# Kernel tuning notes

Measured on AMD Instinct MI355X. Metric: run time of the kernel, lower is better.

Reference implementation:

```python
import jax, jax.numpy as jnp
import numpy as np

N_NODES = 100000
N_EDGES = 1600000
IN_FEATS = 128
HEADS = 4
OUT_FEATS = 32
NEG_SLOPE = 0.2


def setup_inputs() -> dict:
    key = jax.random.key(0)
    ks = jax.random.split(key, 7)
    x = jax.random.normal(ks[0], (N_NODES, IN_FEATS), dtype=jnp.float32)
    fc_w = jax.random.normal(ks[1], (HEADS * OUT_FEATS, IN_FEATS), dtype=jnp.float32) * (1.0 / np.sqrt(IN_FEATS))
    attn_l = jax.random.normal(ks[2], (HEADS, OUT_FEATS), dtype=jnp.float32) * (1.0 / np.sqrt(OUT_FEATS))
    attn_r = jax.random.normal(ks[3], (HEADS, OUT_FEATS), dtype=jnp.float32) * (1.0 / np.sqrt(OUT_FEATS))
    bias = jnp.zeros((HEADS * OUT_FEATS,), dtype=jnp.float32)
    src = jax.random.randint(ks[4], (N_EDGES,), 0, N_NODES, dtype=jnp.int64 if jax.config.jax_enable_x64 else jnp.int32)
    dst = jax.random.randint(ks[5], (N_EDGES,), 0, N_NODES, dtype=jnp.int64 if jax.config.jax_enable_x64 else jnp.int32)
    return {"x": x, "fc_w": fc_w, "attn_l": attn_l, "attn_r": attn_r, "bias": bias, "src": src, "dst": dst}


def reference(x, fc_w, attn_l, attn_r, bias, src, dst):
    """DGL GATConv (feat_drop=attn_drop=0, residual identity since in==H*D,
    allow_zero_in_degree=True, activation=None), then concat heads."""
    N = x.shape[0]
    H, D = attn_l.shape
    # linear projection: [N, H, D]
    feat = (x @ fc_w.T).reshape(N, H, D)
    # per-node attention halves: [N, H]
    el = jnp.einsum('nhd,hd->nh', feat, attn_l)
    er = jnp.einsum('nhd,hd->nh', feat, attn_r)
    # per-edge score with leaky relu: [E, H]
    e = el[src] + er[dst]
    e = jnp.where(e > 0, e, NEG_SLOPE * e)
    # edge softmax grouped by destination node
    emax = jax.ops.segment_max(e, dst, num_segments=N)          # [N, H]
    ee = jnp.exp(e - emax[dst])                                  # [E, H]
    denom = jax.ops.segment_sum(ee, dst, num_segments=N)        # [N, H]
    a = ee / jnp.maximum(denom[dst], jnp.float32(1e-38))         # [E, H]
    # weighted message + scatter aggregate: [N, H, D]
    msg = feat[src] * a[:, :, None]
    rst = jax.ops.segment_sum(msg, dst, num_segments=N)
    # residual (identity since in_feats == H*D) + bias
    rst = rst + x.reshape(N, H, D) + bias.reshape(1, H, D)
    # concat heads
    return rst.reshape(N, H * D)
```

## Files before the change

kernel.cpp:

```cpp
#include <hip/hip_runtime.h>
#include <math.h>

#define NEG_SLOPE 0.2f
#define PB 256
#define BKT_SHIFT 8
#define WSLICES 8

typedef __attribute__((ext_vector_type(8))) short bf16x8;
typedef __attribute__((ext_vector_type(4))) float f32x4;

__device__ __forceinline__ unsigned bf16_rne(float f) {
  unsigned u = __float_as_uint(f);
  return (u + 0x7fff + ((u >> 16) & 1)) >> 16;
}

__device__ __forceinline__ float lrelu_exp(float v) {
  v = v > 0.f ? v : NEG_SLOPE * v;
  return __expf(v);
}

__device__ __forceinline__ void local_blk_scan(const int* __restrict__ blk_sums,
                                               int* s_blk_off, int nb, int t) {
  if (t < 64) {
    const int v = (t < nb) ? blk_sums[t] : 0;
    int incl = v;
#pragma unroll
    for (int d = 1; d < 64; d <<= 1) {
      const int o = __shfl_up(incl, d);
      if (t >= d) incl += o;
    }
    s_blk_off[t] = incl - v;
  }
}

__global__ __launch_bounds__(256) void gemm_feat_attn(
    const float* __restrict__ x, const unsigned* __restrict__ fc_wb,
    const float* __restrict__ attn_l, const float* __restrict__ attn_r,
    unsigned* __restrict__ featb, float* __restrict__ el,
    float* __restrict__ er, int N)
{
  __shared__ __align__(16) unsigned w_lds[128 * 68];
  const int t = threadIdx.x;
  const int row_base = blockIdx.x * 64;

  {
    const uint4* fb4 = reinterpret_cast<const uint4*>(fc_wb);
#pragma unroll
    for (int k = 0; k < 8; ++k) {
      const int i4 = t + k * 256;
      const uint4 v = fb4[i4];
      const int row = i4 >> 4;
      unsigned* d = &w_lds[row * 68 + (i4 & 15) * 4];
      d[0] = v.x; d[1] = v.y; d[2] = v.z; d[3] = v.w;
    }
  }

  const int w = t >> 6;
  const int l = t & 63;
  const int cl = l & 15;
  const int g = l >> 4;

  const int arow = min(row_base + w * 16 + cl, N - 1);
  const float* __restrict__ xp = x + (size_t)arow * 128;
  bf16x8 a_frag[4];
#pragma unroll
  for (int ks = 0; ks < 4; ++ks) {
    const float4 v0 = *reinterpret_cast<const float4*>(xp + ks * 32 + g * 8);
    const float4 v1 =
        *reinterpret_cast<const float4*>(xp + ks * 32 + g * 8 + 4);
    uint4 uu;
    uu.x = bf16_rne(v0.x) | (bf16_rne(v0.y) << 16);
    uu.y = bf16_rne(v0.z) | (bf16_rne(v0.w) << 16);
    uu.z = bf16_rne(v1.x) | (bf16_rne(v1.y) << 16);
    uu.w = bf16_rne(v1.z) | (bf16_rne(v1.w) << 16);
    a_frag[ks] = *reinterpret_cast<bf16x8*>(&uu);
  }
  __syncthreads();

  f32x4 acc[8];
#pragma unroll
  for (int ct = 0; ct < 8; ++ct) acc[ct] = (f32x4){0.f, 0.f, 0.f, 0.f};

#pragma unroll
  for (int ct = 0; ct < 8; ++ct) {
#pragma unroll
    for (int ks = 0; ks < 4; ++ks) {
      const bf16x8 b_frag = *reinterpret_cast<const bf16x8*>(
          &w_lds[(ct * 16 + cl) * 68 + ks * 16 + g * 4]);
      acc[ct] = __builtin_amdgcn_mfma_f32_16x16x32_bf16(a_frag[ks], b_frag,
                                                        acc[ct], 0, 0, 0);
    }
  }

#pragma unroll
  for (int ct = 0; ct < 8; ++ct) {
#pragma unroll
    for (int r = 0; r < 4; ++r) {
      const float v = acc[ct][r];
      const float vn = __shfl_xor(v, 1);
      const int node = row_base + w * 16 + g * 4 + r;
      if ((cl & 1) == 0 && node < N) {
        featb[(size_t)node * 64 + ct * 8 + (cl >> 1)] =
            bf16_rne(v) | (bf16_rne(vn) << 16);
      }
    }
  }

  float al_lo[4], al_hi[4], ar_lo[4], ar_hi[4];
#pragma unroll
  for (int h = 0; h < 4; ++h) {
    al_lo[h] = attn_l[h * 32 + cl];
    al_hi[h] = attn_l[h * 32 + 16 + cl];
    ar_lo[h] = attn_r[h * 32 + cl];
    ar_hi[h] = attn_r[h * 32 + 16 + cl];
  }
#pragma unroll
  for (int r = 0; r < 4; ++r) {
    const int node = row_base + w * 16 + g * 4 + r;
#pragma unroll
    for (int h = 0; h < 4; ++h) {
      float pl = acc[2 * h][r] * al_lo[h] + acc[2 * h + 1][r] * al_hi[h];
      float pr = acc[2 * h][r] * ar_lo[h] + acc[2 * h + 1][r] * ar_hi[h];
#pragma unroll
      for (int d = 1; d < 16; d <<= 1) {
        pl += __shfl_xor(pl, d);
        pr += __shfl_xor(pr, d);
      }
      if (cl == 0 && node < N) {
        el[(size_t)node * 4 + h] = pl;
        er[(size_t)node * 4 + h] = pr;
      }
    }
  }
}

__global__ __launch_bounds__(256) void hist_bucket(const int* __restrict__ dst,
                                                   int* __restrict__ hist,
                                                   const float* __restrict__ fc_w,
                                                   unsigned* __restrict__ fc_wb,
                                                   int E, int NB, int chunk) {
  __shared__ int h[512];
  const int k = blockIdx.x, t = threadIdx.x;
  if (k < 32) {
    const int i = k * 256 + t;
    const float2 v = reinterpret_cast<const float2*>(fc_w)[i];
    fc_wb[i] = bf16_rne(v.x) | (bf16_rne(v.y) << 16);
  }
  for (int i = t; i < NB; i += 256) h[i] = 0;
  __syncthreads();
  const int beg = k * chunk, end = min(E, beg + chunk);
  for (int e = beg + t; e < end; e += 256)
    atomicAdd(&h[dst[e] >> BKT_SHIFT], 1);
  __syncthreads();
  for (int i = t; i < NB; i += 256) hist[i * PB + k] = h[i];
}

__global__ __launch_bounds__(256) void scan_a(const int* __restrict__ deg,
                                              int* __restrict__ offs,
                                              int* __restrict__ blk_sums,
                                              int n) {
  __shared__ int wsum[4];
  const int b = blockIdx.x, t = threadIdx.x;
  const int base = b * 2048 + t * 8;
  int v[8];
  int s = 0;
#pragma unroll
  for (int j = 0; j < 8; ++j) {
    v[j] = s;
    const int d = (base + j < n) ? deg[base + j] : 0;
    s += d;
  }
  const int lane = t & 63;
  int incl = s;
#pragma unroll
  for (int d = 1; d < 64; d <<= 1) {
    const int o = __shfl_up(incl, d);
    if (lane >= d) incl += o;
  }
  const int w = t >> 6;
  if (lane == 63) wsum[w] = incl;
  __syncthreads();
  int woff = 0;
  for (int ww = 0; ww < w; ++ww) woff += wsum[ww];
  const int thr_excl = woff + incl - s;
#pragma unroll
  for (int j = 0; j < 8; ++j)
    if (base + j < n) offs[base + j] = thr_excl + v[j];
  if (t == 255) blk_sums[b] = woff + incl;
}

__global__ __launch_bounds__(256) void part_scatter(
    const int* __restrict__ src, const int* __restrict__ dst,
    const int* __restrict__ hscan, const int* __restrict__ blk_sums,
    unsigned* __restrict__ part, int E, int NB, int chunk, int nb) {
  __shared__ int cur[512];
  __shared__ int s_blk_off[64];
  const int k = blockIdx.x, t = threadIdx.x;
  local_blk_scan(blk_sums, s_blk_off, nb, t);
  __syncthreads();
  for (int i = t; i < NB; i += 256) {
    const int m = i * PB + k;
    cur[i] = hscan[m] + s_blk_off[m >> 11];
  }
  __syncthreads();
  const int beg = k * chunk, end = min(E, beg + chunk);
  for (int e = beg + t; e < end; e += 256) {
    const int d = dst[e];
    const int b = d >> BKT_SHIFT;
    const int pos = atomicAdd(&cur[b], 1);
    part[pos] = (unsigned)src[e] |
                ((unsigned)(d & ((1 << BKT_SHIFT) - 1)) << 20);
  }
}

__global__ __launch_bounds__(256) void build_csr(
    const unsigned* __restrict__ part, const int* __restrict__ hscan,
    const int* __restrict__ blk_sums, int* __restrict__ node_offs,
    unsigned* __restrict__ csr, int N, int E, int NB, int nb) {
  __shared__ int cnt[256];
  __shared__ int wtot[4];
  __shared__ int s_blk_off[64];
  const int b = blockIdx.x, t = threadIdx.x;
  local_blk_scan(blk_sums, s_blk_off, nb, t);
  if (t < 256) cnt[t] = 0;
  __syncthreads();
  const int m0 = b * PB;
  const int bbase = hscan[m0] + s_blk_off[m0 >> 11];
  int bend = E;
  if (b + 1 < NB) {
    const int m1 = (b + 1) * PB;
    bend = hscan[m1] + s_blk_off[m1 >> 11];
  }
  const int node0 = b << BKT_SHIFT;
  for (int p = bbase + t; p < bend; p += 256)
    atomicAdd(&cnt[part[p] >> 20], 1);
  __syncthreads();
  const int a0 = cnt[t];
  int incl = a0;
#pragma unroll
  for (int d1 = 1; d1 < 64; d1 <<= 1) {
    const int o = __shfl_up(incl, d1);
    if ((t & 63) >= d1) incl += o;
  }
  const int w = t >> 6;
  if ((t & 63) == 63) wtot[w] = incl;
  __syncthreads();
  int woff = 0;
  for (int ww = 0; ww < w; ++ww) woff += wtot[ww];
  const int e0 = woff + incl - a0;
  cnt[t] = e0;
  if (node0 + t < N) node_offs[node0 + t] = bbase + e0;
  if (b == NB - 1 && t == 0) node_offs[N] = E;
  __syncthreads();
  for (int p = bbase + t; p < bend; p += 256) {
    const unsigned v = part[p];
    const int lpos = atomicAdd(&cnt[v >> 20], 1);
    csr[bbase + lpos] = v;
  }
}

__global__ __launch_bounds__(256) void compute_w(
    const unsigned* __restrict__ csr, const int* __restrict__ hscan,
    const int* __restrict__ blk_sums, const float* __restrict__ el,
    const float* __restrict__ er, uint2* __restrict__ wsb, int E, int NB,
    int nb) {
  __shared__ int s_blk_off[64];
  const int b = blockIdx.x / WSLICES;
  const int sl = blockIdx.x - b * WSLICES;
  local_blk_scan(blk_sums, s_blk_off, nb, (int)threadIdx.x);
  __syncthreads();
  const int m0 = b * PB;
  const int bbase = hscan[m0] + s_blk_off[m0 >> 11];
  int bend = E;
  if (b + 1 < NB) {
    const int m1 = (b + 1) * PB;
    bend = hscan[m1] + s_blk_off[m1 >> 11];
  }
  const int node0 = b << BKT_SHIFT;
  const int len = bend - bbase;
  const int per = (len + WSLICES - 1) / WSLICES;
  const int s0 = bbase + sl * per;
  const int s1 = min(bend, s0 + per);
  for (int pos = s0 + (int)threadIdx.x; pos < s1; pos += 256) {
    const unsigned v = csr[pos];
    const unsigned s = v & 0xFFFFFu;
    const unsigned ld = v >> 20;
    const float4 l4 = *reinterpret_cast<const float4*>(el + s * 4);
    const float4 r4 =
        *reinterpret_cast<const float4*>(er + (unsigned)(node0 + ld) * 4);
    uint2 u;
    u.x = bf16_rne(lrelu_exp(l4.x + r4.x)) |
          (bf16_rne(lrelu_exp(l4.y + r4.y)) << 16);
    u.y = bf16_rne(lrelu_exp(l4.z + r4.z)) |
          (bf16_rne(lrelu_exp(l4.w + r4.w)) << 16);
    wsb[pos] = u;
  }
}

__global__ __launch_bounds__(256) void agg_kernel(
    const uint2* __restrict__ featb2, const unsigned* __restrict__ csr,
    const unsigned short* __restrict__ wsb_us, const float* __restrict__ x,
    const float* __restrict__ bias, const int* __restrict__ node_offs,
    float* __restrict__ out, int N, int E)
{
  const int n = (int)((blockIdx.x * (size_t)blockDim.x + threadIdx.x) >> 6);
  if (n >= N) return;
  const unsigned lane = threadIdx.x & 63;
  const unsigned half = lane >> 5;
  const unsigned li = lane & 31;
  const unsigned hh = li >> 3;
  const unsigned short* __restrict__ wp = wsb_us + hh;
  const int beg = node_offs[n];
  const int end = node_offs[n + 1];
  const int nfull = (end - beg) >> 3;

  float a0 = 0.f, a1 = 0.f, a2 = 0.f, a3 = 0.f, ds = 0.f;
  int p = beg;
  for (int gi = 0; gi < nfull; ++gi, p += 8) {
    unsigned pk[4]; unsigned wu[4]; uint2 fv[4];
#pragma unroll
    for (int i = 0; i < 4; ++i) pk[i] = csr[(unsigned)p + 2 * i + half];
#pragma unroll
    for (int i = 0; i < 4; ++i)
      wu[i] = wp[((unsigned)p + 2 * i + half) * 4];
#pragma unroll
    for (int i = 0; i < 4; ++i)
      fv[i] = featb2[(pk[i] & 0xFFFFFu) * 32 + li];
#pragma unroll
    for (int i = 0; i < 4; ++i) {
      const float w = __uint_as_float(wu[i] << 16);
      a0 = fmaf(w, __uint_as_float(fv[i].x << 16), a0);
      a1 = fmaf(w, __uint_as_float(fv[i].x & 0xffff0000u), a1);
      a2 = fmaf(w, __uint_as_float(fv[i].y << 16), a2);
      a3 = fmaf(w, __uint_as_float(fv[i].y & 0xffff0000u), a3);
      ds += w;
    }
  }
  if (p < end) {
    const int last = end - 1;
#pragma unroll
    for (int i = 0; i < 4; ++i) {
      const int e = p + 2 * i + (int)half;
      const unsigned ec = (unsigned)min(e, last);
      const unsigned pk = csr[ec];
      float w = __uint_as_float((unsigned)wp[ec * 4] << 16);
      if (e > last) w = 0.f;
      const uint2 fv = featb2[(pk & 0xFFFFFu) * 32 + li];
      a0 = fmaf(w, __uint_as_float(fv.x << 16), a0);
      a1 = fmaf(w, __uint_as_float(fv.x & 0xffff0000u), a1);
      a2 = fmaf(w, __uint_as_float(fv.y << 16), a2);
      a3 = fmaf(w, __uint_as_float(fv.y & 0xffff0000u), a3);
      ds += w;
    }
  }

  a0 += __shfl_xor(a0, 32);
  a1 += __shfl_xor(a1, 32);
  a2 += __shfl_xor(a2, 32);
  a3 += __shfl_xor(a3, 32);
  ds += __shfl_xor(ds, 32);

  if (half == 0) {
    const float inv = 1.f / fmaxf(ds, 1e-38f);
    const float4 xr = ((const float4*)x)[(unsigned)n * 32 + li];
    const float4 br = ((const float4*)bias)[li];
    float4 o;
    o.x = fmaf(a0, inv, xr.x + br.x);
    o.y = fmaf(a1, inv, xr.y + br.y);
    o.z = fmaf(a2, inv, xr.z + br.z);
    o.w = fmaf(a3, inv, xr.w + br.w);
    ((float4*)out)[(unsigned)n * 32 + li] = o;
  }
}

extern "C" void kernel_launch(void* const* d_in, const int* in_sizes, int n_in,
                              void* d_out, int out_size, void* d_ws,
                              size_t ws_size, hipStream_t stream) {
  const float* x      = (const float*)d_in[0];
  const float* fc_w   = (const float*)d_in[1];
  const float* attn_l = (const float*)d_in[2];
  const float* attn_r = (const float*)d_in[3];
  const float* bias   = (const float*)d_in[4];
  const int*   src    = (const int*)d_in[5];
  const int*   dst    = (const int*)d_in[6];
  const int N = in_sizes[0] / 128;
  const int E = in_sizes[5];
  float* out = (float*)d_out;

  const int NB = (N + 255) >> 8;
  const int M = NB * PB;
  const int chunk = (E + PB - 1) / PB;
  const int nb = (M + 2047) / 2048;

  char* ws = (char*)d_ws;
  size_t off = 0;
  auto alloc = [&](size_t bytes) {
    void* p = ws + off;
    off += (bytes + 255) & ~(size_t)255;
    return p;
  };
  unsigned* featb   = (unsigned*)alloc((size_t)N * 128 * 2);
  unsigned* fc_wb   = (unsigned*)alloc(128 * 64 * 4);
  float* el         = (float*)alloc((size_t)N * 4 * 4);
  float* er         = (float*)alloc((size_t)N * 4 * 4);
  int*   hist       = (int*)alloc((size_t)M * 4);
  int*   hscan      = (int*)alloc((size_t)(M + 1) * 4);
  int*   node_offs  = (int*)alloc((size_t)(N + 1) * 4);
  int*   blk_sums   = (int*)alloc(256);
  unsigned* part    = (unsigned*)alloc((size_t)E * 4);
  unsigned* csr     = (unsigned*)alloc((size_t)E * 4);
  uint2* wsb        = (uint2*)alloc((size_t)E * 8);

  hist_bucket<<<PB, 256, 0, stream>>>(dst, hist, fc_w, fc_wb, E, NB, chunk);
  gemm_feat_attn<<<(N + 63) / 64, 256, 0, stream>>>(x, fc_wb, attn_l, attn_r,
                                                    featb, el, er, N);
  scan_a<<<nb, 256, 0, stream>>>(hist, hscan, blk_sums, M);
  part_scatter<<<PB, 256, 0, stream>>>(src, dst, hscan, blk_sums, part, E,
                                       NB, chunk, nb);
  build_csr<<<NB, 256, 0, stream>>>(part, hscan, blk_sums, node_offs, csr, N,
                                    E, NB, nb);
  compute_w<<<NB * WSLICES, 256, 0, stream>>>(csr, hscan, blk_sums, el, er,
                                              wsb, E, NB, nb);
  agg_kernel<<<(N + 3) / 4, 256, 0, stream>>>((const uint2*)featb, csr,
                                              (const unsigned short*)wsb, x,
                                              bias, node_offs, out, N, E);
}
```

Measured before the change: 159.7 us.

## Fuse edge-weight computation into CSR build and widen aggregation feature loads

Removes the separate compute_w kernel by computing the bf16 exp-weights inside build_csr, which now runs with 512 threads per block and re-reads csr after a barrier. The aggregation kernel switches from 32-lane uint2 feature loads (2 edges per wave step) to 16-lane uint4 loads (4 edges per step), with an extra shuffle stage for the reduction. This saves one launch plus the global re-read of bucket offsets and reduces load instructions per edge. In exchange, build_csr gets less parallelism per bucket (391 blocks instead of 3128 for the weight pass), and the accumulators in aggregation use more registers.

```diff
diff --git a/kernel.cpp b/kernel.cpp
--- a/kernel.cpp
+++ b/kernel.cpp
@@ -4,7 +4,6 @@
 #define NEG_SLOPE 0.2f
 #define PB 256
 #define BKT_SHIFT 8
-#define WSLICES 8
 
 typedef __attribute__((ext_vector_type(8))) short bf16x8;
 typedef __attribute__((ext_vector_type(4))) float f32x4;
@@ -213,10 +212,12 @@
   }
 }
 
-__global__ __launch_bounds__(256) void build_csr(
+__global__ __launch_bounds__(512) void build_csr(
     const unsigned* __restrict__ part, const int* __restrict__ hscan,
-    const int* __restrict__ blk_sums, int* __restrict__ node_offs,
-    unsigned* __restrict__ csr, int N, int E, int NB, int nb) {
+    const int* __restrict__ blk_sums, const float* __restrict__ el,
+    const float* __restrict__ er, int* __restrict__ node_offs,
+    unsigned* __restrict__ csr, uint2* __restrict__ wsb,
+    int N, int E, int NB, int nb) {
   __shared__ int cnt[256];
   __shared__ int wtot[4];
   __shared__ int s_blk_off[64];
@@ -232,57 +233,39 @@
     bend = hscan[m1] + s_blk_off[m1 >> 11];
   }
   const int node0 = b << BKT_SHIFT;
-  for (int p = bbase + t; p < bend; p += 256)
+  for (int p = bbase + t; p < bend; p += 512)
     atomicAdd(&cnt[part[p] >> 20], 1);
   __syncthreads();
-  const int a0 = cnt[t];
-  int incl = a0;
-#pragma unroll
-  for (int d1 = 1; d1 < 64; d1 <<= 1) {
-    const int o = __shfl_up(incl, d1);
-    if ((t & 63) >= d1) incl += o;
-  }
-  const int w = t >> 6;
-  if ((t & 63) == 63) wtot[w] = incl;
-  __syncthreads();
-  int woff = 0;
-  for (int ww = 0; ww < w; ++ww) woff += wtot[ww];
-  const int e0 = woff + incl - a0;
-  cnt[t] = e0;
-  if (node0 + t < N) node_offs[node0 + t] = bbase + e0;
-  if (b == NB - 1 && t == 0) node_offs[N] = E;
-  __syncthreads();
-  for (int p = bbase + t; p < bend; p += 256) {
+  int a0 = 0, incl = 0;
+  if (t < 256) {
+    a0 = cnt[t];
+    incl = a0;
+#pragma unroll
+    for (int d1 = 1; d1 < 64; d1 <<= 1) {
+      const int o = __shfl_up(incl, d1);
+      if ((t & 63) >= d1) incl += o;
+    }
+    if ((t & 63) == 63) wtot[t >> 6] = incl;
+  }
+  __syncthreads();
+  if (t < 256) {
+    const int w = t >> 6;
+    int woff = 0;
+    for (int ww = 0; ww < w; ++ww) woff += wtot[ww];
+    const int e0 = woff + incl - a0;
+    cnt[t] = e0;
+    if (node0 + t < N) node_offs[node0 + t] = bbase + e0;
+    if (b == NB - 1 && t == 0) node_offs[N] = E;
+  }
+  __syncthreads();
+  for (int p = bbase + t; p < bend; p += 512) {
     const unsigned v = part[p];
     const int lpos = atomicAdd(&cnt[v >> 20], 1);
     csr[bbase + lpos] = v;
   }
-}
-
-__global__ __launch_bounds__(256) void compute_w(
-    const unsigned* __restrict__ csr, const int* __restrict__ hscan,
-    const int* __restrict__ blk_sums, const float* __restrict__ el,
-    const float* __restrict__ er, uint2* __restrict__ wsb, int E, int NB,
-    int nb) {
-  __shared__ int s_blk_off[64];
-  const int b = blockIdx.x / WSLICES;
-  const int sl = blockIdx.x - b * WSLICES;
-  local_blk_scan(blk_sums, s_blk_off, nb, (int)threadIdx.x);
-  __syncthreads();
-  const int m0 = b * PB;
-  const int bbase = hscan[m0] + s_blk_off[m0 >> 11];
-  int bend = E;
-  if (b + 1 < NB) {
-    const int m1 = (b + 1) * PB;
-    bend = hscan[m1] + s_blk_off[m1 >> 11];
-  }
-  const int node0 = b << BKT_SHIFT;
-  const int len = bend - bbase;
-  const int per = (len + WSLICES - 1) / WSLICES;
-  const int s0 = bbase + sl * per;
-  const int s1 = min(bend, s0 + per);
-  for (int pos = s0 + (int)threadIdx.x; pos < s1; pos += 256) {
-    const unsigned v = csr[pos];
+  __syncthreads();
+  for (int p = bbase + t; p < bend; p += 512) {
+    const unsigned v = csr[p];
     const unsigned s = v & 0xFFFFFu;
     const unsigned ld = v >> 20;
     const float4 l4 = *reinterpret_cast<const float4*>(el + s * 4);
@@ -293,12 +276,12 @@
           (bf16_rne(lrelu_exp(l4.y + r4.y)) << 16);
     u.y = bf16_rne(lrelu_exp(l4.z + r4.z)) |
           (bf16_rne(lrelu_exp(l4.w + r4.w)) << 16);
-    wsb[pos] = u;
+    wsb[p] = u;
   }
 }
 
 __global__ __launch_bounds__(256) void agg_kernel(
-    const uint2* __restrict__ featb2, const unsigned* __restrict__ csr,
+    const uint4* __restrict__ featb4, const unsigned* __restrict__ csr,
     const unsigned short* __restrict__ wsb_us, const float* __restrict__ x,
     const float* __restrict__ bias, const int* __restrict__ node_offs,
     float* __restrict__ out, int N, int E)
@@ -306,70 +289,90 @@
   const int n = (int)((blockIdx.x * (size_t)blockDim.x + threadIdx.x) >> 6);
   if (n >= N) return;
   const unsigned lane = threadIdx.x & 63;
-  const unsigned half = lane >> 5;
-  const unsigned li = lane & 31;
-  const unsigned hh = li >> 3;
+  const unsigned q = lane >> 4;
+  const unsigned li = lane & 15;
+  const unsigned hh = li >> 2;
   const unsigned short* __restrict__ wp = wsb_us + hh;
   const int beg = node_offs[n];
   const int end = node_offs[n + 1];
   const int nfull = (end - beg) >> 3;
 
-  float a0 = 0.f, a1 = 0.f, a2 = 0.f, a3 = 0.f, ds = 0.f;
+  float a0 = 0.f, a1 = 0.f, a2 = 0.f, a3 = 0.f;
+  float a4 = 0.f, a5 = 0.f, a6 = 0.f, a7 = 0.f, ds = 0.f;
   int p = beg;
   for (int gi = 0; gi < nfull; ++gi, p += 8) {
-    unsigned pk[4]; unsigned wu[4]; uint2 fv[4];
-#pragma unroll
-    for (int i = 0; i < 4; ++i) pk[i] = csr[(unsigned)p + 2 * i + half];
-#pragma unroll
-    for (int i = 0; i < 4; ++i)
-      wu[i] = wp[((unsigned)p + 2 * i + half) * 4];
-#pragma unroll
-    for (int i = 0; i < 4; ++i)
-      fv[i] = featb2[(pk[i] & 0xFFFFFu) * 32 + li];
-#pragma unroll
-    for (int i = 0; i < 4; ++i) {
+    unsigned pk[2]; unsigned wu[2]; uint4 fv[2];
+#pragma unroll
+    for (int i = 0; i < 2; ++i) pk[i] = csr[(unsigned)p + 4 * i + q];
+#pragma unroll
+    for (int i = 0; i < 2; ++i)
+      wu[i] = wp[((unsigned)p + 4 * i + q) * 4];
+#pragma unroll
+    for (int i = 0; i < 2; ++i)
+      fv[i] = featb4[(pk[i] & 0xFFFFFu) * 16 + li];
+#pragma unroll
+    for (int i = 0; i < 2; ++i) {
       const float w = __uint_as_float(wu[i] << 16);
       a0 = fmaf(w, __uint_as_float(fv[i].x << 16), a0);
       a1 = fmaf(w, __uint_as_float(fv[i].x & 0xffff0000u), a1);
       a2 = fmaf(w, __uint_as_float(fv[i].y << 16), a2);
       a3 = fmaf(w, __uint_as_float(fv[i].y & 0xffff0000u), a3);
+      a4 = fmaf(w, __uint_as_float(fv[i].z << 16), a4);
+      a5 = fmaf(w, __uint_as_float(fv[i].z & 0xffff0000u), a5);
+      a6 = fmaf(w, __uint_as_float(fv[i].w << 16), a6);
+      a7 = fmaf(w, __uint_as_float(fv[i].w & 0xffff0000u), a7);
       ds += w;
     }
   }
   if (p < end) {
     const int last = end - 1;
 #pragma unroll
-    for (int i = 0; i < 4; ++i) {
-      const int e = p + 2 * i + (int)half;
+    for (int i = 0; i < 2; ++i) {
+      const int e = p + 4 * i + (int)q;
       const unsigned ec = (unsigned)min(e, last);
       const unsigned pk = csr[ec];
       float w = __uint_as_float((unsigned)wp[ec * 4] << 16);
       if (e > last) w = 0.f;
-      const uint2 fv = featb2[(pk & 0xFFFFFu) * 32 + li];
+      const uint4 fv = featb4[(pk & 0xFFFFFu) * 16 + li];
       a0 = fmaf(w, __uint_as_float(fv.x << 16), a0);
       a1 = fmaf(w, __uint_as_float(fv.x & 0xffff0000u), a1);
       a2 = fmaf(w, __uint_as_float(fv.y << 16), a2);
       a3 = fmaf(w, __uint_as_float(fv.y & 0xffff0000u), a3);
+      a4 = fmaf(w, __uint_as_float(fv.z << 16), a4);
+      a5 = fmaf(w, __uint_as_float(fv.z & 0xffff0000u), a5);
+      a6 = fmaf(w, __uint_as_float(fv.w << 16), a6);
+      a7 = fmaf(w, __uint_as_float(fv.w & 0xffff0000u), a7);
       ds += w;
     }
   }
 
-  a0 += __shfl_xor(a0, 32);
-  a1 += __shfl_xor(a1, 32);
-  a2 += __shfl_xor(a2, 32);
-  a3 += __shfl_xor(a3, 32);
-  ds += __shfl_xor(ds, 32);
-
-  if (half == 0) {
+  a0 += __shfl_xor(a0, 16); a0 += __shfl_xor(a0, 32);
+  a1 += __shfl_xor(a1, 16); a1 += __shfl_xor(a1, 32);
+  a2 += __shfl_xor(a2, 16); a2 += __shfl_xor(a2, 32);
+  a3 += __shfl_xor(a3, 16); a3 += __shfl_xor(a3, 32);
+  a4 += __shfl_xor(a4, 16); a4 += __shfl_xor(a4, 32);
+  a5 += __shfl_xor(a5, 16); a5 += __shfl_xor(a5, 32);
+  a6 += __shfl_xor(a6, 16); a6 += __shfl_xor(a6, 32);
+  a7 += __shfl_xor(a7, 16); a7 += __shfl_xor(a7, 32);
+  ds += __shfl_xor(ds, 16); ds += __shfl_xor(ds, 32);
+
+  if (q == 0) {
     const float inv = 1.f / fmaxf(ds, 1e-38f);
-    const float4 xr = ((const float4*)x)[(unsigned)n * 32 + li];
-    const float4 br = ((const float4*)bias)[li];
-    float4 o;
-    o.x = fmaf(a0, inv, xr.x + br.x);
-    o.y = fmaf(a1, inv, xr.y + br.y);
-    o.z = fmaf(a2, inv, xr.z + br.z);
-    o.w = fmaf(a3, inv, xr.w + br.w);
-    ((float4*)out)[(unsigned)n * 32 + li] = o;
+    const float4 x0 = ((const float4*)x)[(unsigned)n * 32 + 2 * li];
+    const float4 x1 = ((const float4*)x)[(unsigned)n * 32 + 2 * li + 1];
+    const float4 b0 = ((const float4*)bias)[2 * li];
+    const float4 b1 = ((const float4*)bias)[2 * li + 1];
+    float4 o0, o1;
+    o0.x = fmaf(a0, inv, x0.x + b0.x);
+    o0.y = fmaf(a1, inv, x0.y + b0.y);
+    o0.z = fmaf(a2, inv, x0.z + b0.z);
+    o0.w = fmaf(a3, inv, x0.w + b0.w);
+    o1.x = fmaf(a4, inv, x1.x + b1.x);
+    o1.y = fmaf(a5, inv, x1.y + b1.y);
+    o1.z = fmaf(a6, inv, x1.z + b1.z);
+    o1.w = fmaf(a7, inv, x1.w + b1.w);
+    ((float4*)out)[(unsigned)n * 32 + 2 * li] = o0;
+    ((float4*)out)[(unsigned)n * 32 + 2 * li + 1] = o1;
   }
 }
 
@@ -417,11 +420,9 @@
   scan_a<<<nb, 256, 0, stream>>>(hist, hscan, blk_sums, M);
   part_scatter<<<PB, 256, 0, stream>>>(src, dst, hscan, blk_sums, part, E,
                                        NB, chunk, nb);
-  build_csr<<<NB, 256, 0, stream>>>(part, hscan, blk_sums, node_offs, csr, N,
-                                    E, NB, nb);
-  compute_w<<<NB * WSLICES, 256, 0, stream>>>(csr, hscan, blk_sums, el, er,
-                                              wsb, E, NB, nb);
-  agg_kernel<<<(N + 3) / 4, 256, 0, stream>>>((const uint2*)featb, csr,
+  build_csr<<<NB, 512, 0, stream>>>(part, hscan, blk_sums, el, er, node_offs,
+                                    csr, wsb, N, E, NB, nb);
+  agg_kernel<<<(N + 3) / 4, 256, 0, stream>>>((const uint4*)featb, csr,
                                               (const unsigned short*)wsb, x,
                                               bias, node_offs, out, N, E);
 }
```

Result: faster. 154.9 us (-3.0%).
